# Optimization experiments

Measured on AMD Instinct MI355X. Metric: run time of the kernel, lower is better.

## Reference

```python
import jax, jax.numpy as jnp
import numpy as np

EPS = 1e-6

def elu_feature_map(x):
    return jax.nn.elu(x) + 1.0

def setup_inputs() -> dict:
    key = jax.random.key(0)
    kq, kk, kv = jax.random.split(key, 3)
    N, L, S, H, D = 8, 8192, 8192, 8, 32
    return {
        "queries": jax.random.normal(kq, (N, L, H, D), dtype=jnp.float32),
        "keys": jax.random.normal(kk, (N, S, H, D), dtype=jnp.float32),
        "values": jax.random.normal(kv, (N, S, H, D), dtype=jnp.float32),
    }

def reference(queries, keys, values):
    # Linear (kernelized) attention, default path of MixAttention.forward
    Q = elu_feature_map(queries)            # [N,L,H,D]
    K = elu_feature_map(keys)               # [N,S,H,D]
    v_length = values.shape[1]
    vals = values / v_length                # [N,S,H,D]
    KV = jnp.einsum('nshd,nshv->nhdv', K, vals)          # [N,H,D,D]
    Z = 1.0 / (jnp.einsum('nlhd,nhd->nlh', Q, K.sum(axis=1)) + EPS)  # [N,L,H]
    out = jnp.einsum('nlhd,nhdv,nlh->nlhv', Q, KV, Z) * v_length     # [N,L,H,D]
    return out
```

## Files before the change

kernel.cpp:

```cpp
#include <hip/hip_runtime.h>


constexpr int N_ = 8, L_ = 8192, S_ = 8192, H_ = 8, D_ = 32;
constexpr int NH = N_ * H_;
constexpr int SPLIT = 16;
constexpr int CS = S_ / SPLIT;
constexpr int PART_STRIDE = D_ * D_ + D_;
constexpr int LCH = 512;
constexpr float EPS_ = 1e-6f;
constexpr int HD = H_ * D_;

__device__ __forceinline__ float fmap(float x) {
    return x > 0.0f ? x + 1.0f : __expf(x);
}

__global__ __launch_bounds__(256, 4) void lin_attn_phase1(
        const float* __restrict__ Kg, const float* __restrict__ Vg,
        float* __restrict__ part) {
    const int blk = blockIdx.x;
    const int nh = blk / SPLIT;
    const int sc = blk % SPLIT;
    const int n = nh / H_, h = nh % H_;
    const int t = threadIdx.x;
    const int w = t >> 6;
    const int j = t & 63;
    const int half = j >> 5;
    const int jj = j & 31;
    const int d0 = (jj & 7) << 2;
    const int v0 = (jj >> 3) << 3;

    __shared__ __align__(16) float red[4][1024];
    __shared__ __align__(16) float ksum_red[4][32];

    float acc[4][8];
    #pragma unroll
    for (int a = 0; a < 4; ++a)
        #pragma unroll
        for (int b = 0; b < 8; ++b) acc[a][b] = 0.0f;
    float kp[4] = {0.f, 0.f, 0.f, 0.f};

    const size_t base = (size_t)n * S_ * H_ * D_ + (size_t)h * D_;
    const int s0 = sc * CS;
    const float* kr = Kg + base + (size_t)(s0 + (w << 1) + half) * HD + d0;
    const float* vr = Vg + base + (size_t)(s0 + (w << 1) + half) * HD + v0;
    constexpr int STRIDE = 8 * HD;

#define BEAT(kq, va, vb) do {                                                  \
        float kd[4];                                                           \
        kd[0] = fmap((kq).x); kd[1] = fmap((kq).y);                            \
        kd[2] = fmap((kq).z); kd[3] = fmap((kq).w);                            \
        kp[0] += kd[0]; kp[1] += kd[1]; kp[2] += kd[2]; kp[3] += kd[3];        \
        const float vs[8] = {(va).x, (va).y, (va).z, (va).w,                   \
                             (vb).x, (vb).y, (vb).z, (vb).w};                  \
        _Pragma("unroll")                                                      \
        for (int a = 0; a < 4; ++a)                                            \
            _Pragma("unroll")                                                  \
            for (int bb = 0; bb < 8; ++bb)                                     \
                acc[a][bb] += kd[a] * vs[bb];                                  \
    } while (0)

    float4 kqA = *reinterpret_cast<const float4*>(kr);
    float4 vaA = *reinterpret_cast<const float4*>(vr);
    float4 vbA = *reinterpret_cast<const float4*>(vr + 4);
    float4 kqB = *reinterpret_cast<const float4*>(kr + STRIDE);
    float4 vaB = *reinterpret_cast<const float4*>(vr + STRIDE);
    float4 vbB = *reinterpret_cast<const float4*>(vr + STRIDE + 4);
    kr += 2 * STRIDE; vr += 2 * STRIDE;

    #pragma unroll 1
    for (int b = 0; b < (CS / 8 - 2) / 2; ++b) {
        float4 kqn = *reinterpret_cast<const float4*>(kr);
        float4 van = *reinterpret_cast<const float4*>(vr);
        float4 vbn = *reinterpret_cast<const float4*>(vr + 4);
        BEAT(kqA, vaA, vbA);
        kqA = kqn; vaA = van; vbA = vbn;
        kqn = *reinterpret_cast<const float4*>(kr + STRIDE);
        van = *reinterpret_cast<const float4*>(vr + STRIDE);
        vbn = *reinterpret_cast<const float4*>(vr + STRIDE + 4);
        BEAT(kqB, vaB, vbB);
        kqB = kqn; vaB = van; vbB = vbn;
        kr += 2 * STRIDE; vr += 2 * STRIDE;
    }
    BEAT(kqA, vaA, vbA);
    BEAT(kqB, vaB, vbB);
#undef BEAT

    #pragma unroll
    for (int a = 0; a < 4; ++a)
        #pragma unroll
        for (int bb = 0; bb < 8; ++bb)
            acc[a][bb] += __shfl_xor(acc[a][bb], 32);
    #pragma unroll
    for (int a = 0; a < 4; ++a) kp[a] += __shfl_xor(kp[a], 32);

    if (j < 32) {
        #pragma unroll
        for (int a = 0; a < 4; ++a) {
            *reinterpret_cast<float4*>(&red[w][(d0 + a) * D_ + v0]) =
                make_float4(acc[a][0], acc[a][1], acc[a][2], acc[a][3]);
            *reinterpret_cast<float4*>(&red[w][(d0 + a) * D_ + v0 + 4]) =
                make_float4(acc[a][4], acc[a][5], acc[a][6], acc[a][7]);
        }
        if (j < 8)
            *reinterpret_cast<float4*>(&ksum_red[w][j << 2]) =
                make_float4(kp[0], kp[1], kp[2], kp[3]);
    }
    __syncthreads();

    float* P = part + ((size_t)sc * NH + nh) * PART_STRIDE;
    const int i4 = t << 2;
    float4 s = make_float4(0.f, 0.f, 0.f, 0.f);
    #pragma unroll
    for (int w2 = 0; w2 < 4; ++w2) {
        const float4 rr = *reinterpret_cast<const float4*>(&red[w2][i4]);
        s.x += rr.x; s.y += rr.y; s.z += rr.z; s.w += rr.w;
    }
    *reinterpret_cast<float4*>(&P[i4]) = s;
    if (t < D_) {
        float ks = 0.f;
        #pragma unroll
        for (int w2 = 0; w2 < 4; ++w2) ks += ksum_red[w2][t];
        P[D_ * D_ + t] = ks;
    }
}

__global__ __launch_bounds__(256) void lin_attn_reduce(
        const float* __restrict__ part, float* __restrict__ red) {
    const int i = blockIdx.x * 256 + threadIdx.x;
    if (i >= NH * PART_STRIDE) return;
    float s = 0.0f;
    #pragma unroll
    for (int sc = 0; sc < SPLIT; ++sc)
        s += part[(size_t)sc * (NH * PART_STRIDE) + i];
    red[i] = s;
}

__global__ __launch_bounds__(256) void lin_attn_phase2(
        const float* __restrict__ Qg, const float* __restrict__ red,
        float* __restrict__ outg) {
    constexpr int QTS = 32;
    constexpr int NLC = L_ / LCH;
    const int nh  = blockIdx.x / NLC;
    const int lcb = blockIdx.x % NLC;
    const int n = nh / H_, h = nh % H_;
    const int t = threadIdx.x;
    const int v  = t & 31;
    const int rb = t >> 5;
    const int r  = t >> 3;
    const int c  = (t & 7) << 2;

    __shared__ __align__(16) float Qt[QTS][D_];

    float kv[D_];
    float ks[D_];
    {
        const float* W = red + (size_t)nh * PART_STRIDE;
        #pragma unroll
        for (int d = 0; d < D_; ++d) kv[d] = W[d * D_ + v];
        #pragma unroll
        for (int d = 0; d < D_; ++d) ks[d] = W[D_ * D_ + d];
    }

    const size_t base = (size_t)n * L_ * H_ * D_ + (size_t)h * D_;
    const int l0 = lcb * LCH;
    for (int step = 0; step < LCH; step += QTS) {
        const float4 q4 = *reinterpret_cast<const float4*>(
            Qg + base + (size_t)(l0 + step + r) * (H_ * D_) + c);
        __syncthreads();
        float4 qf;
        qf.x = fmap(q4.x); qf.y = fmap(q4.y);
        qf.z = fmap(q4.z); qf.w = fmap(q4.w);
        *reinterpret_cast<float4*>(&Qt[r][c]) = qf;
        __syncthreads();
        #pragma unroll
        for (int rr = 0; rr < 4; ++rr) {
            const int row = (rr << 3) + rb;
            float acc = 0.0f, accz = 0.0f;
            #pragma unroll
            for (int d = 0; d < D_; ++d) {
                const float q = Qt[row][d];
                acc  += q * kv[d];
                accz += q * ks[d];
            }
            outg[base + (size_t)(l0 + step + row) * (H_ * D_) + v] =
                acc / (accz + EPS_);
        }
    }
}

extern "C" void kernel_launch(void* const* d_in, const int* in_sizes, int n_in,
                              void* d_out, int out_size, void* d_ws, size_t ws_size,
                              hipStream_t stream) {
    const float* Q = (const float*)d_in[0];
    const float* K = (const float*)d_in[1];
    const float* V = (const float*)d_in[2];
    float* out  = (float*)d_out;
    float* part = (float*)d_ws;
    float* red  = part + (size_t)SPLIT * NH * PART_STRIDE;

    lin_attn_phase1<<<NH * SPLIT, 256, 0, stream>>>(K, V, part);
    lin_attn_reduce<<<(NH * PART_STRIDE + 255) / 256, 256, 0, stream>>>(part, red);
    lin_attn_phase2<<<NH * (L_ / LCH), 256, 0, stream>>>(Q, red, out);
}
```

Measured before the change: 90.64 us.

## Deepen phase1 load prefetch and compute normalizer once per row in phase2

Phase 1 now keeps four rows of K/V loads in flight instead of two, so more memory latency is hidden per wave. The cost is more live registers. Phase 2 computes each row's normalizer once, using a shuffle reduction during the Q tile load, and stores its reciprocal in shared memory. This removes the redundant per-thread ksum dot product and the division. The inner loop also reads Q from shared memory as float2. These changes cut ALU work and LDS traffic, at the cost of one extra shared array and a multiply by a reciprocal instead of a true division.

```diff
diff --git a/kernel.cpp b/kernel.cpp
--- a/kernel.cpp
+++ b/kernel.cpp
@@ -59,30 +59,29 @@
                 acc[a][bb] += kd[a] * vs[bb];                                  \
     } while (0)
 
-    float4 kqA = *reinterpret_cast<const float4*>(kr);
-    float4 vaA = *reinterpret_cast<const float4*>(vr);
-    float4 vbA = *reinterpret_cast<const float4*>(vr + 4);
-    float4 kqB = *reinterpret_cast<const float4*>(kr + STRIDE);
-    float4 vaB = *reinterpret_cast<const float4*>(vr + STRIDE);
-    float4 vbB = *reinterpret_cast<const float4*>(vr + STRIDE + 4);
-    kr += 2 * STRIDE; vr += 2 * STRIDE;
+#define LOAD(s) do {                                                           \
+        kq##s = *reinterpret_cast<const float4*>(kr + (s) * STRIDE);           \
+        va##s = *reinterpret_cast<const float4*>(vr + (s) * STRIDE);           \
+        vb##s = *reinterpret_cast<const float4*>(vr + (s) * STRIDE + 4);       \
+    } while (0)
+
+    float4 kq0, va0, vb0, kq1, va1, vb1, kq2, va2, vb2, kq3, va3, vb3;
+    LOAD(0); LOAD(1); LOAD(2); LOAD(3);
+    kr += 4 * STRIDE; vr += 4 * STRIDE;
 
     #pragma unroll 1
-    for (int b = 0; b < (CS / 8 - 2) / 2; ++b) {
-        float4 kqn = *reinterpret_cast<const float4*>(kr);
-        float4 van = *reinterpret_cast<const float4*>(vr);
-        float4 vbn = *reinterpret_cast<const float4*>(vr + 4);
-        BEAT(kqA, vaA, vbA);
-        kqA = kqn; vaA = van; vbA = vbn;
-        kqn = *reinterpret_cast<const float4*>(kr + STRIDE);
-        van = *reinterpret_cast<const float4*>(vr + STRIDE);
-        vbn = *reinterpret_cast<const float4*>(vr + STRIDE + 4);
-        BEAT(kqB, vaB, vbB);
-        kqB = kqn; vaB = van; vbB = vbn;
-        kr += 2 * STRIDE; vr += 2 * STRIDE;
-    }
-    BEAT(kqA, vaA, vbA);
-    BEAT(kqB, vaB, vbB);
+    for (int b = 0; b < (CS / 8 - 4) / 4; ++b) {
+        BEAT(kq0, va0, vb0); LOAD(0);
+        BEAT(kq1, va1, vb1); LOAD(1);
+        BEAT(kq2, va2, vb2); LOAD(2);
+        BEAT(kq3, va3, vb3); LOAD(3);
+        kr += 4 * STRIDE; vr += 4 * STRIDE;
+    }
+    BEAT(kq0, va0, vb0);
+    BEAT(kq1, va1, vb1);
+    BEAT(kq2, va2, vb2);
+    BEAT(kq3, va3, vb3);
+#undef LOAD
 #undef BEAT
 
     #pragma unroll
@@ -150,16 +149,13 @@
     const int c  = (t & 7) << 2;
 
     __shared__ __align__(16) float Qt[QTS][D_];
+    __shared__ float zinv_sh[QTS];
 
     float kv[D_];
-    float ks[D_];
-    {
-        const float* W = red + (size_t)nh * PART_STRIDE;
-        #pragma unroll
-        for (int d = 0; d < D_; ++d) kv[d] = W[d * D_ + v];
-        #pragma unroll
-        for (int d = 0; d < D_; ++d) ks[d] = W[D_ * D_ + d];
-    }
+    const float* W = red + (size_t)nh * PART_STRIDE;
+    #pragma unroll
+    for (int d = 0; d < D_; ++d) kv[d] = W[d * D_ + v];
+    const float4 ksq = *reinterpret_cast<const float4*>(W + D_ * D_ + c);
 
     const size_t base = (size_t)n * L_ * H_ * D_ + (size_t)h * D_;
     const int l0 = lcb * LCH;
@@ -171,19 +167,23 @@
         qf.x = fmap(q4.x); qf.y = fmap(q4.y);
         qf.z = fmap(q4.z); qf.w = fmap(q4.w);
         *reinterpret_cast<float4*>(&Qt[r][c]) = qf;
+        float zp = qf.x * ksq.x + qf.y * ksq.y + qf.z * ksq.z + qf.w * ksq.w;
+        zp += __shfl_xor(zp, 1);
+        zp += __shfl_xor(zp, 2);
+        zp += __shfl_xor(zp, 4);
+        if ((t & 7) == 0) zinv_sh[r] = 1.0f / (zp + EPS_);
         __syncthreads();
         #pragma unroll
         for (int rr = 0; rr < 4; ++rr) {
             const int row = (rr << 3) + rb;
-            float acc = 0.0f, accz = 0.0f;
+            float acc = 0.0f;
             #pragma unroll
-            for (int d = 0; d < D_; ++d) {
-                const float q = Qt[row][d];
-                acc  += q * kv[d];
-                accz += q * ks[d];
+            for (int d2 = 0; d2 < 16; ++d2) {
+                const float2 q = *reinterpret_cast<const float2*>(&Qt[row][d2 << 1]);
+                acc += q.x * kv[(d2 << 1)] + q.y * kv[(d2 << 1) + 1];
             }
             outg[base + (size_t)(l0 + step + row) * (H_ * D_) + v] =
-                acc / (accz + EPS_);
+                acc * zinv_sh[row];
         }
     }
 }
```

After: 182.5 us. +101.3%, slower.
